# Kernel tuning notes

Hardware: AMD Instinct MI355X
Metric: run time of the kernel (lower is better)

The kernel has to match this reference:

```python
import jax, jax.numpy as jnp
import numpy as np

N, IN_F, OUT_F, H = 4096, 256, 512, 8
D = OUT_F // H  # hidden per head
NEG_SLOPE = 0.2


def setup_inputs() -> dict:
    key = jax.random.key(0)
    k1, k2, k3 = jax.random.split(key, 3)
    inp = jax.random.normal(k1, (N, IN_F), dtype=jnp.float32)
    A = jnp.zeros((N, N), dtype=jnp.float32)  # additive adjacency mask
    # xavier_uniform for W [out, in]
    limW = float(np.sqrt(6.0 / (IN_F + H * D)))
    W = jax.random.uniform(k2, (H * D, IN_F), minval=-limW, maxval=limW, dtype=jnp.float32)
    lima = float(np.sqrt(6.0 / (H * D + 1)))
    a_left = jax.random.uniform(k3, (1, H, D), minval=-lima, maxval=lima, dtype=jnp.float32)
    return {"inp": inp, "A": A, "W": W, "a_left": a_left}


def reference(inp, A, W, a_left):
    # h: [N, H, D]
    h = (inp @ W.T).reshape(-1, H, D)
    # NOTE: source uses a_left for BOTH source and target scores (a_right is dead code)
    scores = jnp.sum(h * a_left, axis=-1)  # [N, H]
    s = scores.T  # [H, N]
    # [H, N, N] additive attention logits
    logits = jax.nn.leaky_relu(s[:, :, None] + s[:, None, :], negative_slope=NEG_SLOPE)
    logits = logits + A[None, :, :]
    att = jax.nn.softmax(logits, axis=-1)  # [H, N, N]
    # bmm: [H,N,N] x [H,N,D] -> [H,N,D] -> [N,H,D]
    out = jnp.einsum('hij,jhd->ihd', att, h)
    return out.reshape(-1, H * D)
```

## Files before the change

kernel.cpp:

```cpp
#include <hip/hip_runtime.h>
#include <hip/hip_bf16.h>
#include <math.h>

#define N 4096
#define IN_F 256
#define OUT_F 512
#define H 8
#define D 64
#define NEG 0.2f
#define LOG2E 1.44269504f

typedef __attribute__((ext_vector_type(8))) short bf16x8;
typedef __attribute__((ext_vector_type(4))) float f32x4;

__device__ __forceinline__ float leaky(float x) { return fmaxf(x, NEG * x); }

__device__ __forceinline__ unsigned short f2bf(float x) {
    union { float f; unsigned u; } v; v.f = x;
    unsigned r = v.u + 0x7fff + ((v.u >> 16) & 1);
    return (unsigned short)(r >> 16);
}

__device__ __forceinline__ unsigned pk_bf16(float a, float b) {
    __hip_bfloat162 h2 = __float22bfloat162_rn(float2{a, b});
    union { __hip_bfloat162 h; unsigned u; } u; u.h = h2;
    return u.u;
}

__device__ __forceinline__ unsigned fmap(float x) {
    union { float f; unsigned u; } v; v.f = x;
    return (v.u & 0x80000000u) ? ~v.u : (v.u | 0x80000000u);
}
__device__ __forceinline__ float funmap(unsigned m) {
    union { float f; unsigned u; } v;
    v.u = (m & 0x80000000u) ? (m & 0x7fffffffu) : ~m;
    return v.f;
}

__device__ __forceinline__ void dma16(const void* g, void* l) {
    __builtin_amdgcn_global_load_lds((const __attribute__((address_space(1))) void*)g,
                                     (__attribute__((address_space(3))) void*)l, 16, 0, 0);
}

__global__ __launch_bounds__(256) void k_gemm(const float* __restrict__ inp,
                                              const float* __restrict__ W,
                                              const float* __restrict__ a_left,
                                              unsigned short* __restrict__ hbT,
                                              float* __restrict__ s,
                                              unsigned* __restrict__ smaxU) {
    __shared__ float As[64][69];
    __shared__ float Bs[64][69];
    __shared__ unsigned short h_st[64][72];
    __shared__ float s_red[64];

    const int t = threadIdx.x;
    const int bi = blockIdx.x;
    const int head = blockIdx.y;
    const int ty = t >> 4, tx = t & 15;
    const int lr = t >> 2;
    const int cq = (t & 3) * 16;

    float4 pa[4], pb[4];
    auto loadrk = [&](int k0) {
        const float* ip = &inp[(size_t)(bi * 64 + lr) * IN_F + k0 + cq];
        const float* wp = &W[(size_t)(head * 64 + lr) * IN_F + k0 + cq];
#pragma unroll
        for (int q = 0; q < 4; ++q) {
            pa[q] = *(const float4*)&ip[q * 4];
            pb[q] = *(const float4*)&wp[q * 4];
        }
    };
    loadrk(0);

    float acc[4][4] = {};
    for (int k0 = 0; k0 < IN_F; k0 += 64) {
        __syncthreads();
#pragma unroll
        for (int q = 0; q < 4; ++q)
#pragma unroll
            for (int j = 0; j < 4; ++j) {
                As[cq + q * 4 + j][lr] = ((const float*)&pa[q])[j];
                Bs[cq + q * 4 + j][lr] = ((const float*)&pb[q])[j];
            }
        __syncthreads();
        if (k0 + 64 < IN_F) loadrk(k0 + 64);
#pragma unroll
        for (int k = 0; k < 64; ++k) {
            float4 a4 = *(const float4*)&As[k][ty * 4];
            float4 b4 = *(const float4*)&Bs[k][tx * 4];
            float a[4] = {a4.x, a4.y, a4.z, a4.w};
            float b[4] = {b4.x, b4.y, b4.z, b4.w};
#pragma unroll
            for (int r = 0; r < 4; ++r)
#pragma unroll
                for (int c = 0; c < 4; ++c) acc[r][c] = fmaf(a[r], b[c], acc[r][c]);
        }
    }

    float aL[4];
#pragma unroll
    for (int c = 0; c < 4; ++c) aL[c] = a_left[head * D + tx * 4 + c];
#pragma unroll
    for (int r = 0; r < 4; ++r) {
        float sp = acc[r][0] * aL[0] + acc[r][1] * aL[1] + acc[r][2] * aL[2] + acc[r][3] * aL[3];
        sp += __shfl_xor(sp, 1); sp += __shfl_xor(sp, 2);
        sp += __shfl_xor(sp, 4); sp += __shfl_xor(sp, 8);
        if (tx == 0) {
            s[head * N + bi * 64 + ty * 4 + r] = sp;
            s_red[ty * 4 + r] = sp;
        }
    }
    __syncthreads();
    if (t < 64) {
        float m = s_red[t];
        for (int off = 32; off; off >>= 1) m = fmaxf(m, __shfl_down(m, off, 64));
        if (t == 0) atomicMax(&smaxU[head], fmap(m));
    }

#pragma unroll
    for (int r = 0; r < 4; ++r) {
        ushort4 v;
        v.x = f2bf(acc[r][0]); v.y = f2bf(acc[r][1]);
        v.z = f2bf(acc[r][2]); v.w = f2bf(acc[r][3]);
        *(ushort4*)&h_st[ty * 4 + r][tx * 4] = v;
    }
    __syncthreads();
    {
        const int d = t >> 2, iq = (t & 3) * 16;
        unsigned short us[16];
#pragma unroll
        for (int k = 0; k < 16; ++k) us[k] = h_st[iq + k][d];
        unsigned short* dst = &hbT[((size_t)(head * D + d)) * N + bi * 64 + iq];
#pragma unroll
        for (int q = 0; q < 4; ++q) {
            ushort4 v = {us[q * 4 + 0], us[q * 4 + 1], us[q * 4 + 2], us[q * 4 + 3]};
            *(ushort4*)&dst[q * 4] = v;
        }
    }
}

__global__ __launch_bounds__(256) void k_rowmax(const float* __restrict__ A,
                                                float* __restrict__ rmax) {
    int i = blockIdx.x;
    const float* row = &A[(size_t)i * N];
    float m = -1e30f;
    for (int j = threadIdx.x * 4; j < N; j += 256 * 4) {
        float4 v = *(const float4*)&row[j];
        m = fmaxf(fmaxf(fmaxf(m, v.x), fmaxf(v.y, v.z)), v.w);
    }
    for (int off = 32; off; off >>= 1) m = fmaxf(m, __shfl_down(m, off, 64));
    __shared__ float red[4];
    if ((threadIdx.x & 63) == 0) red[threadIdx.x >> 6] = m;
    __syncthreads();
    if (threadIdx.x == 0) rmax[i] = fmaxf(fmaxf(red[0], red[1]), fmaxf(red[2], red[3]));
}

__global__ __launch_bounds__(512, 4) void k_attn(const float* __restrict__ A,
                                                 const unsigned short* __restrict__ hbT,
                                                 const float* __restrict__ s,
                                                 const unsigned* __restrict__ smaxU,
                                                 const float* __restrict__ rmax,
                                                 float* __restrict__ out) {
    __shared__ unsigned short hT_st[2][16384];

    const int t = threadIdx.x;
    const int bid = blockIdx.x;
    const int hg = bid & 1;
    const int i0 = (bid >> 1) * 16;

    const int lane = t & 63, wave = t >> 6;
    const int quad = lane >> 4, li = lane & 15;
    const int wh = wave & 3, jh = wave >> 2;
    const int head = hg * 4 + wh;
    const int row = i0 + li;
    const int jb = jh * 2048;
    const int NSTEP = 2048 / 32;
    const int wbase = wave * 2048;

    const float sr = s[head * N + row];
    const float sI = sr * LOG2E;
    const float mb = (leaky(sr + funmap(smaxU[head])) + rmax[row]) * LOG2E;

    const unsigned short* gH[4];
#pragma unroll
    for (int q = 0; q < 4; ++q) {
        int m = q * 64 + lane, Rloc = m >> 2, sl = m & 3;
        int grow = head * 64 + Rloc;
        int jcol = jb + ((sl ^ ((Rloc >> 1) & 3)) * 8);
        gH[q] = &hbT[(size_t)grow * N + jcol];
    }

    const float* Ap = &A[(size_t)row * N + jb + quad * 8];
    const float* sp = &s[(size_t)head * N + jb + quad * 8];

    f32x4 acc[4] = {{0,0,0,0},{0,0,0,0},{0,0,0,0},{0,0,0,0}};
    f32x4 acc_z = {0, 0, 0, 0};
    bf16x8 vones;
#pragma unroll
    for (int k = 0; k < 8; ++k) vones[k] = (short)0x3F80;

    const int hsw = quad ^ ((li >> 1) & 3);

    auto issue_tile = [&](int buf, int jn) {
#pragma unroll
        for (int q = 0; q < 4; ++q)
            dma16(gH[q] + jn, &hT_st[buf][wbase + (q * 64 + lane) * 8]);
    };

    float4 rA0[4], rA1[4], rS0[4], rS1[4];
#define LOAD_AS(SET, JN)                                                   \
    do {                                                                   \
        rA0[SET] = *(const float4*)&Ap[(JN)];                              \
        rA1[SET] = *(const float4*)&Ap[(JN) + 4];                          \
        rS0[SET] = *(const float4*)&sp[(JN)];                              \
        rS1[SET] = *(const float4*)&sp[(JN) + 4];                          \
    } while (0)

    auto compute_tile = [&](int buf, float4 A0, float4 A1, float4 S0, float4 S1) {
        float av[8] = {A0.x, A0.y, A0.z, A0.w, A1.x, A1.y, A1.z, A1.w};
        float sv[8] = {S0.x, S0.y, S0.z, S0.w, S1.x, S1.y, S1.z, S1.w};
        union { bf16x8 v; unsigned u[4]; } P;
#pragma unroll
        for (int p = 0; p < 4; ++p) {
            float x0 = fmaf(sv[2 * p + 0], LOG2E, sI);
            float x1 = fmaf(sv[2 * p + 1], LOG2E, sI);
            float w0 = __builtin_amdgcn_exp2f(fmaxf(x0, NEG * x0) + fmaf(av[2 * p + 0], LOG2E, -mb));
            float w1 = __builtin_amdgcn_exp2f(fmaxf(x1, NEG * x1) + fmaf(av[2 * p + 1], LOG2E, -mb));
            P.u[p] = pk_bf16(w0, w1);
        }
        acc_z = __builtin_amdgcn_mfma_f32_16x16x32_bf16(P.v, vones, acc_z, 0, 0, 0);
        const unsigned short* bH = &hT_st[buf][wbase];
#pragma unroll
        for (int db = 0; db < 4; ++db) {
            const int d = db * 16 + li;
            bf16x8 hf = *(const bf16x8*)&bH[(d * 4 + hsw) * 8];
            acc[db] = __builtin_amdgcn_mfma_f32_16x16x32_bf16(P.v, hf, acc[db], 0, 0, 0);
        }
    };

#define WAIT12 asm volatile("s_waitcnt vmcnt(12)" ::: "memory")
#define WAIT8  asm volatile("s_waitcnt vmcnt(8)"  ::: "memory")
#define WAIT0  asm volatile("s_waitcnt vmcnt(0)"  ::: "memory")
#define SBAR   __builtin_amdgcn_sched_barrier(0)

    issue_tile(0, 0);
    LOAD_AS(0, 0);
    LOAD_AS(1, 32);

#pragma unroll 1
    for (int itp = 0; itp < NSTEP / 4 - 1; ++itp) {
#pragma unroll
        for (int u = 0; u < 4; ++u) {
            const int t4 = itp * 4 + u;
            issue_tile((u + 1) & 1, (t4 + 1) * 32);
            {
                const int jn = (t4 + 2) * 32;
                switch ((u + 2) & 3) {
                    case 0: LOAD_AS(0, jn); break;
                    case 1: LOAD_AS(1, jn); break;
                    case 2: LOAD_AS(2, jn); break;
                    case 3: LOAD_AS(3, jn); break;
                }
            }
            WAIT12; SBAR;
            compute_tile(u & 1, rA0[u], rA1[u], rS0[u], rS1[u]);
        }
    }
    issue_tile(1, 61 * 32); LOAD_AS(2, 62 * 32);
    WAIT12; SBAR;
    compute_tile(0, rA0[0], rA1[0], rS0[0], rS1[0]);

    issue_tile(0, 62 * 32); LOAD_AS(3, 63 * 32);
    WAIT12; SBAR;
    compute_tile(1, rA0[1], rA1[1], rS0[1], rS1[1]);

    issue_tile(1, 63 * 32);
    WAIT8; SBAR;
    compute_tile(0, rA0[2], rA1[2], rS0[2], rS1[2]);

    WAIT0; SBAR;
    compute_tile(1, rA0[3], rA1[3], rS0[3], rS1[3]);

#undef LOAD_AS
#undef WAIT12
#undef WAIT8
#undef WAIT0
#undef SBAR

    __syncthreads();
    float* red = (float*)&hT_st[0][0];
    if (jh == 1) {
        const int base = (wh * 64 + lane) * 21;
#pragma unroll
        for (int db = 0; db < 4; ++db)
#pragma unroll
            for (int r = 0; r < 4; ++r) red[base + db * 4 + r] = acc[db][r];
#pragma unroll
        for (int r = 0; r < 4; ++r) red[base + 16 + r] = acc_z[r];
    }
    __syncthreads();
    if (jh == 0) {
        const int base = (wh * 64 + lane) * 21;
#pragma unroll
        for (int db = 0; db < 4; ++db)
#pragma unroll
            for (int r = 0; r < 4; ++r) acc[db][r] += red[base + db * 4 + r];
#pragma unroll
        for (int r = 0; r < 4; ++r) {
            const float zT = acc_z[r] + red[base + 16 + r];
            const float inv = 1.0f / zT;
            float* op = &out[(size_t)(i0 + quad * 4 + r) * OUT_F + head * D];
#pragma unroll
            for (int db = 0; db < 4; ++db) op[db * 16 + li] = acc[db][r] * inv;
        }
    }
}

extern "C" void kernel_launch(void* const* d_in, const int* in_sizes, int n_in,
                              void* d_out, int out_size, void* d_ws, size_t ws_size,
                              hipStream_t stream) {
    const float* inp = (const float*)d_in[0];
    const float* A = (const float*)d_in[1];
    const float* W = (const float*)d_in[2];
    const float* a_left = (const float*)d_in[3];
    float* out = (float*)d_out;

    unsigned short* hbT = (unsigned short*)d_ws;
    float* s = (float*)((char*)d_ws + (size_t)H * D * N * 2);
    unsigned* smaxU = (unsigned*)(s + (size_t)H * N);
    float* rmax = (float*)(smaxU + 8);

    hipMemsetAsync(smaxU, 0, 8 * sizeof(unsigned), stream);

    k_gemm<<<dim3(N / 64, H), 256, 0, stream>>>(inp, W, a_left, hbT, s, smaxU);
    k_rowmax<<<dim3(N), 256, 0, stream>>>(A, rmax);
    k_attn<<<dim3((N / 16) * 2), 512, 0, stream>>>(A, hbT, s, smaxU, rmax, out);
}
```

Baseline: 245.3 us.

## Retile projection GEMM to 512 threads and split attention into four launches

The projection GEMM moves from 256 to 512 threads per block. Each thread now computes a 2x4 output tile instead of 4x4, with new load mappings and reworked transposed-store indexing. This is meant to raise occupancy and latency hiding for the small GEMM. The attention kernel gains a block-offset argument and is issued as four sequential 128-block launches instead of one 512-block launch. That adds launch overhead, and each launch may leave many compute units idle because same-stream launches serialize.

```diff
diff --git a/kernel.cpp b/kernel.cpp
--- a/kernel.cpp
+++ b/kernel.cpp
@@ -42,56 +42,56 @@
                                      (__attribute__((address_space(3))) void*)l, 16, 0, 0);
 }
 
-__global__ __launch_bounds__(256) void k_gemm(const float* __restrict__ inp,
-                                              const float* __restrict__ W,
-                                              const float* __restrict__ a_left,
-                                              unsigned short* __restrict__ hbT,
-                                              float* __restrict__ s,
-                                              unsigned* __restrict__ smaxU) {
-    __shared__ float As[64][69];
-    __shared__ float Bs[64][69];
+__global__ __launch_bounds__(512, 4) void k_gemm(const float* __restrict__ inp,
+                                                 const float* __restrict__ W,
+                                                 const float* __restrict__ a_left,
+                                                 unsigned short* __restrict__ hbT,
+                                                 float* __restrict__ s,
+                                                 unsigned* __restrict__ smaxU) {
+    __shared__ float As[64][70];
+    __shared__ float Bs[64][68];
     __shared__ unsigned short h_st[64][72];
     __shared__ float s_red[64];
 
     const int t = threadIdx.x;
     const int bi = blockIdx.x;
     const int head = blockIdx.y;
-    const int ty = t >> 4, tx = t & 15;
-    const int lr = t >> 2;
-    const int cq = (t & 3) * 16;
-
-    float4 pa[4], pb[4];
+    const int ty = t >> 4;
+    const int tx = t & 15;
+    const int lrA = t >> 3;
+    const int cqA = (t & 7) * 8;
+    const int lrB = t & 63;
+    const int cqB = (t >> 6) * 8;
+
+    float4 pa[2], pb[2];
     auto loadrk = [&](int k0) {
-        const float* ip = &inp[(size_t)(bi * 64 + lr) * IN_F + k0 + cq];
-        const float* wp = &W[(size_t)(head * 64 + lr) * IN_F + k0 + cq];
-#pragma unroll
-        for (int q = 0; q < 4; ++q) {
-            pa[q] = *(const float4*)&ip[q * 4];
-            pb[q] = *(const float4*)&wp[q * 4];
-        }
+        const float* ip = &inp[(size_t)(bi * 64 + lrA) * IN_F + k0 + cqA];
+        const float* wp = &W[(size_t)(head * 64 + lrB) * IN_F + k0 + cqB];
+        pa[0] = *(const float4*)&ip[0]; pa[1] = *(const float4*)&ip[4];
+        pb[0] = *(const float4*)&wp[0]; pb[1] = *(const float4*)&wp[4];
     };
     loadrk(0);
 
-    float acc[4][4] = {};
+    float acc[2][4] = {};
     for (int k0 = 0; k0 < IN_F; k0 += 64) {
         __syncthreads();
 #pragma unroll
-        for (int q = 0; q < 4; ++q)
+        for (int q = 0; q < 2; ++q)
 #pragma unroll
             for (int j = 0; j < 4; ++j) {
-                As[cq + q * 4 + j][lr] = ((const float*)&pa[q])[j];
-                Bs[cq + q * 4 + j][lr] = ((const float*)&pb[q])[j];
+                As[cqA + q * 4 + j][lrA] = ((const float*)&pa[q])[j];
+                Bs[cqB + q * 4 + j][lrB] = ((const float*)&pb[q])[j];
             }
         __syncthreads();
         if (k0 + 64 < IN_F) loadrk(k0 + 64);
 #pragma unroll
         for (int k = 0; k < 64; ++k) {
-            float4 a4 = *(const float4*)&As[k][ty * 4];
+            float2 a2 = *(const float2*)&As[k][ty * 2];
             float4 b4 = *(const float4*)&Bs[k][tx * 4];
-            float a[4] = {a4.x, a4.y, a4.z, a4.w};
+            float a[2] = {a2.x, a2.y};
             float b[4] = {b4.x, b4.y, b4.z, b4.w};
 #pragma unroll
-            for (int r = 0; r < 4; ++r)
+            for (int r = 0; r < 2; ++r)
 #pragma unroll
                 for (int c = 0; c < 4; ++c) acc[r][c] = fmaf(a[r], b[c], acc[r][c]);
         }
@@ -101,13 +101,13 @@
 #pragma unroll
     for (int c = 0; c < 4; ++c) aL[c] = a_left[head * D + tx * 4 + c];
 #pragma unroll
-    for (int r = 0; r < 4; ++r) {
+    for (int r = 0; r < 2; ++r) {
         float sp = acc[r][0] * aL[0] + acc[r][1] * aL[1] + acc[r][2] * aL[2] + acc[r][3] * aL[3];
         sp += __shfl_xor(sp, 1); sp += __shfl_xor(sp, 2);
         sp += __shfl_xor(sp, 4); sp += __shfl_xor(sp, 8);
         if (tx == 0) {
-            s[head * N + bi * 64 + ty * 4 + r] = sp;
-            s_red[ty * 4 + r] = sp;
+            s[head * N + bi * 64 + ty * 2 + r] = sp;
+            s_red[ty * 2 + r] = sp;
         }
     }
     __syncthreads();
@@ -118,21 +118,21 @@
     }
 
 #pragma unroll
-    for (int r = 0; r < 4; ++r) {
+    for (int r = 0; r < 2; ++r) {
         ushort4 v;
         v.x = f2bf(acc[r][0]); v.y = f2bf(acc[r][1]);
         v.z = f2bf(acc[r][2]); v.w = f2bf(acc[r][3]);
-        *(ushort4*)&h_st[ty * 4 + r][tx * 4] = v;
+        *(ushort4*)&h_st[ty * 2 + r][tx * 4] = v;
     }
     __syncthreads();
     {
-        const int d = t >> 2, iq = (t & 3) * 16;
-        unsigned short us[16];
-#pragma unroll
-        for (int k = 0; k < 16; ++k) us[k] = h_st[iq + k][d];
+        const int d = t >> 3, iq = (t & 7) * 8;
+        unsigned short us[8];
+#pragma unroll
+        for (int k = 0; k < 8; ++k) us[k] = h_st[iq + k][d];
         unsigned short* dst = &hbT[((size_t)(head * D + d)) * N + bi * 64 + iq];
 #pragma unroll
-        for (int q = 0; q < 4; ++q) {
+        for (int q = 0; q < 2; ++q) {
             ushort4 v = {us[q * 4 + 0], us[q * 4 + 1], us[q * 4 + 2], us[q * 4 + 3]};
             *(ushort4*)&dst[q * 4] = v;
         }
@@ -160,11 +160,12 @@
                                                  const float* __restrict__ s,
                                                  const unsigned* __restrict__ smaxU,
                                                  const float* __restrict__ rmax,
-                                                 float* __restrict__ out) {
+                                                 float* __restrict__ out,
+                                                 int bid0) {
     __shared__ unsigned short hT_st[2][16384];
 
     const int t = threadIdx.x;
-    const int bid = blockIdx.x;
+    const int bid = blockIdx.x + bid0;
     const int hg = bid & 1;
     const int i0 = (bid >> 1) * 16;
 
@@ -332,7 +333,8 @@
 
     hipMemsetAsync(smaxU, 0, 8 * sizeof(unsigned), stream);
 
-    k_gemm<<<dim3(N / 64, H), 256, 0, stream>>>(inp, W, a_left, hbT, s, smaxU);
+    k_gemm<<<dim3(N / 64, H), 512, 0, stream>>>(inp, W, a_left, hbT, s, smaxU);
     k_rowmax<<<dim3(N), 256, 0, stream>>>(A, rmax);
-    k_attn<<<dim3((N / 16) * 2), 512, 0, stream>>>(A, hbT, s, smaxU, rmax, out);
-}
+    for (int q = 0; q < 4; ++q)
+        k_attn<<<dim3(128), 512, 0, stream>>>(A, hbT, s, smaxU, rmax, out, q * 128);
+}
```

Result: slower. 351.1 us (+43.1%).
